# Optimization experiments

Hardware: AMD Instinct MI355X
Metric: run time of the kernel (lower is better)

Reference implementation:

```python
import jax, jax.numpy as jnp
import numpy as np

FG_THRESH = 0.5

def _descriptors(fmap, scribbles):
    # fmap: [B, C, h, w]; scribbles: [B, I, H, W]
    B, C, h, w = fmap.shape
    I = scribbles.shape[1]
    # bilinear resize (align_corners=False == half-pixel, no antialias, like torch)
    sr = jax.image.resize(scribbles, (B, I, h, w), method='bilinear', antialias=False)
    mask = (sr > FG_THRESH).astype(fmap.dtype)                 # [B, I, h, w]
    cnt = mask.sum(axis=(-1, -2))                              # [B, I]
    ssum = jnp.einsum('bihw,bchw->bic', mask, fmap)            # masked sum over HW
    mean = ssum / jnp.maximum(cnt, 1.0)[..., None]             # [B, I, C]
    # fallback when a mask has no foreground pixels: feature at argmax of soft mask
    idx = jnp.argmax(sr.reshape(B, I, h * w), axis=-1)         # [B, I]
    fflat = fmap.reshape(B, C, h * w)
    fb = jnp.take_along_axis(fflat, idx[:, None, :], axis=2)   # [B, C, I]
    fb = fb.transpose(0, 2, 1)                                 # [B, I, C]
    return jnp.where((cnt > 0)[..., None], mean, fb)

def setup_inputs() -> dict:
    key = jax.random.key(0)
    k0, k1, k2, k3 = jax.random.split(key, 4)
    return {
        'feat0': jax.random.normal(k0, (8, 256, 128, 128), dtype=jnp.float32),
        'feat1': jax.random.normal(k1, (8, 256, 64, 64), dtype=jnp.float32),
        'feat2': jax.random.normal(k2, (8, 256, 32, 32), dtype=jnp.float32),
        'scribbles': jax.random.uniform(k3, (8, 16, 512, 512), dtype=jnp.float32),
    }

def reference(feat0, feat1, feat2, scribbles):
    # multi_scale=True, random_bg_queries=False: per-level masked mean pool,
    # then average descriptors across feature levels. Output: [B, I, C]
    d0 = _descriptors(feat0, scribbles)
    d1 = _descriptors(feat1, scribbles)
    d2 = _descriptors(feat2, scribbles)
    return (d0 + d1 + d2) / 3.0
```

## Files before the change

### kernel.cpp

```cpp
#include <hip/hip_runtime.h>
#include <stdint.h>

#define NB 8
#define NI 16
#define NC 256
#define SH 512
#define NCH 84

typedef __bf16 bf16x8 __attribute__((ext_vector_type(8)));
typedef float f32x4 __attribute__((ext_vector_type(4)));
typedef uint32_t u32x4 __attribute__((ext_vector_type(4)));

static const size_t OFF_SSP = 0;
static const size_t OFF_CNT = OFF_SSP + (size_t)NB * NCH * NI * NC * 4;
static const size_t OFF_KEY = OFF_CNT + (size_t)NB * NCH * NI * 4;
static const size_t WS_NEED = OFF_KEY + (size_t)NB * NCH * NI * 8;

__device__ __forceinline__ float4 ld4(const float* p) {
    return *reinterpret_cast<const float4*>(p);
}

__device__ __forceinline__ void mfma_step1(const uint16_t* __restrict__ lmp, int ks, int cl,
                                           const float4 (&buf)[2], f32x4& a0) {
    const uint4 wA = *reinterpret_cast<const uint4*>(lmp + ks * 32);
    u32x4 au;
    au.x = ((wA.x >> cl) & 0x10001u) * 0x3F80u;
    au.y = ((wA.y >> cl) & 0x10001u) * 0x3F80u;
    au.z = ((wA.z >> cl) & 0x10001u) * 0x3F80u;
    au.w = ((wA.w >> cl) & 0x10001u) * 0x3F80u;
    const bf16x8 av = __builtin_bit_cast(bf16x8, au);
    bf16x8 bv;
    bv[0] = (__bf16)buf[0].x; bv[1] = (__bf16)buf[0].y;
    bv[2] = (__bf16)buf[0].z; bv[3] = (__bf16)buf[0].w;
    bv[4] = (__bf16)buf[1].x; bv[5] = (__bf16)buf[1].y;
    bv[6] = (__bf16)buf[1].z; bv[7] = (__bf16)buf[1].w;
    a0 = __builtin_amdgcn_mfma_f32_16x16x32_bf16(av, bv, a0, 0, 0, 0);
}

template<int W, int S, int P>
__device__ __forceinline__ void do_chunk(const float* __restrict__ f,
                                         const float* __restrict__ scr,
                                         float* __restrict__ ssp,
                                         int* __restrict__ cntp,
                                         unsigned long long* __restrict__ keyp,
                                         int b, int chunk, int slot, int tid,
                                         uint8_t* __restrict__ lmask8,
                                         uint16_t* __restrict__ lmask16,
                                         int* __restrict__ lcnt,
                                         unsigned long long* __restrict__ lkey) {
    const int wave = tid >> 6;
    const int lane = tid & 63;
    const int kg = lane >> 4;
    const int cl = lane & 15;
    const int c0 = wave * 16;
    const int kb = chunk * 256;
    const float* fp0 = f + ((size_t)b * NC + c0 + cl) * P + kb + kg * 8;
    float4 bA[2], bB[2];
    bA[0] = ld4(fp0);
    bA[1] = ld4(fp0 + 4);

    const int gi = tid >> 8;
    const int p = tid & 255;
    const int pix = chunk * 256 + p;
    const int y = pix / W;
    const int x = pix - y * W;
    const int r0 = S * y + (S / 2 - 1);
    const int c0s = S * x + (S / 2 - 1);
    const float* sb = scr + ((size_t)b * NI + gi * 4) * (SH * SH) + (size_t)r0 * SH;
    float s4v[4];
    if constexpr (S == 4) {
        float4 q0[4], q1[4];
        #pragma unroll
        for (int i = 0; i < 4; ++i) {
            const float* sp = sb + (size_t)i * (SH * SH);
            q0[i] = ld4(sp + (c0s - 1));
            q1[i] = ld4(sp + SH + (c0s - 1));
        }
        #pragma unroll
        for (int i = 0; i < 4; ++i)
            s4v[i] = (q0[i].y + q0[i].z) + (q1[i].y + q1[i].z);
    } else {
        float qa[4], qb[4], qc[4], qd[4];
        #pragma unroll
        for (int i = 0; i < 4; ++i) {
            const float* sp = sb + (size_t)i * (SH * SH);
            qa[i] = sp[c0s];
            qb[i] = sp[c0s + 1];
            qc[i] = sp[SH + c0s];
            qd[i] = sp[SH + c0s + 1];
        }
        #pragma unroll
        for (int i = 0; i < 4; ++i)
            s4v[i] = (qa[i] + qb[i]) + (qc[i] + qd[i]);
    }
    unsigned int mword = 0;
    #pragma unroll
    for (int i = 0; i < 4; ++i) {
        const float s4 = s4v[i];
        bool bit = s4 > 2.0f;
        mword |= bit ? (1u << i) : 0u;
        unsigned long long bal = __ballot(bit);
        if (lane == 0) atomicAdd(&lcnt[gi * 4 + i], (int)__popcll(bal));
        if (bal == 0ull) {
            unsigned int srb = __float_as_uint(0.25f * s4);
            unsigned int mx = srb;
            #pragma unroll
            for (int off = 1; off < 64; off <<= 1) {
                unsigned int o = __shfl_xor(mx, off, 64);
                mx = (o > mx) ? o : mx;
            }
            unsigned long long win = __ballot(srb == mx);
            if (lane == 0) {
                int wl = __ffsll((unsigned long long)win) - 1;
                unsigned int wpix = (unsigned int)(chunk * 256 + (p & ~63) + wl);
                unsigned long long key = (((unsigned long long)mx) << 32)
                                       | (unsigned long long)(0xFFFFFFFFu - wpix);
                atomicMax(&lkey[gi * 4 + i], key);
            }
        }
    }
    lmask8[gi * 256 + p] = (uint8_t)mword;
    __syncthreads();
    if (tid < 256)
        lmask16[tid] = (uint16_t)((unsigned)lmask8[tid]
                                | ((unsigned)lmask8[256 + tid] << 4)
                                | ((unsigned)lmask8[512 + tid] << 8)
                                | ((unsigned)lmask8[768 + tid] << 12));
    if (tid < NI) {
        cntp[slot * NI + tid] = lcnt[tid];
        keyp[slot * NI + tid] = lkey[tid];
    }
    __syncthreads();

    const uint16_t* lmp = lmask16 + kg * 8;
    f32x4 acc = {0.f, 0.f, 0.f, 0.f};
    #pragma unroll
    for (int ks = 0; ks < 8; ks += 2) {
        {
            const float* fr = fp0 + (ks + 1) * 32;
            bB[0] = ld4(fr);
            bB[1] = ld4(fr + 4);
        }
        mfma_step1(lmp, ks, cl, bA, acc);
        if (ks + 2 < 8) {
            const float* fr = fp0 + (ks + 2) * 32;
            bA[0] = ld4(fr);
            bA[1] = ld4(fr + 4);
        }
        mfma_step1(lmp, ks + 1, cl, bB, acc);
    }
    float* sb2 = ssp + (size_t)slot * (NI * NC);
    const int c = c0 + cl;
    #pragma unroll
    for (int r = 0; r < 4; ++r)
        sb2[(kg * 4 + r) * NC + c] = acc[r];
}

__global__ __launch_bounds__(1024, 8) void fused_kernel(const float* __restrict__ f0,
                                                        const float* __restrict__ f1,
                                                        const float* __restrict__ f2,
                                                        const float* __restrict__ scr,
                                                        float* __restrict__ ssp,
                                                        int* __restrict__ cntp,
                                                        unsigned long long* __restrict__ keyp) {
    __shared__ uint8_t lmask8[1024];
    __shared__ __align__(16) uint16_t lmask16[256];
    __shared__ int lcnt[NI];
    __shared__ unsigned long long lkey[NI];
    const int tid = threadIdx.x;
    const int b = blockIdx.y;
    const int bx = blockIdx.x;
    if (tid < NI) { lcnt[tid] = 0; lkey[tid] = 0ull; }
    __syncthreads();
    const int slot = b * NCH + bx;
    if (bx < 64) {
        do_chunk<128, 4, 16384>(f0, scr, ssp, cntp, keyp, b, bx, slot, tid,
                                lmask8, lmask16, lcnt, lkey);
    } else if (bx < 80) {
        do_chunk<64, 8, 4096>(f1, scr, ssp, cntp, keyp, b, bx - 64, slot, tid,
                              lmask8, lmask16, lcnt, lkey);
    } else {
        do_chunk<32, 16, 1024>(f2, scr, ssp, cntp, keyp, b, bx - 80, slot, tid,
                               lmask8, lmask16, lcnt, lkey);
    }
}

__global__ __launch_bounds__(256) void final_kernel(const float* __restrict__ f0,
                                                    const float* __restrict__ f1,
                                                    const float* __restrict__ f2,
                                                    const int* __restrict__ cntp,
                                                    const unsigned long long* __restrict__ keyp,
                                                    const float* __restrict__ ssp,
                                                    float* __restrict__ out) {
    __shared__ int scnt[3];
    __shared__ unsigned long long skey[3];
    __shared__ float red[4][64];
    const int bi = blockIdx.x;
    const int cq = blockIdx.y;
    const int b = bi >> 4;
    const int i = bi & 15;
    const int tid = threadIdx.x;
    const int cl = tid & 63;
    const int jg = tid >> 6;
    const int CH[3] = {64, 16, 4};
    const int O[3] = {0, 64, 80};
    if (tid < 3) { scnt[tid] = 0; skey[tid] = 0ull; }
    __syncthreads();
    if (tid < NCH) {
        int l = (tid < 64) ? 0 : (tid < 80) ? 1 : 2;
        const int slot = b * NCH + tid;
        atomicAdd(&scnt[l], cntp[slot * NI + i]);
        atomicMax(&skey[l], keyp[slot * NI + i]);
    }
    __syncthreads();
    const float* fl[3] = {f0, f1, f2};
    const int Ps[3] = {16384, 4096, 1024};
    float r = 0.f;
    #pragma unroll
    for (int l = 0; l < 3; ++l) {
        const int cn = scnt[l];
        if (cn > 0) {
            float s = 0.f;
            for (int j = jg; j < CH[l]; j += 4)
                s += ssp[((size_t)(b * NCH + O[l] + j) * NI + i) * NC + cq * 64 + cl];
            red[jg][cl] = s;
            __syncthreads();
            if (jg == 0)
                r += ((red[0][cl] + red[1][cl]) + (red[2][cl] + red[3][cl])) / (float)cn;
            __syncthreads();
        } else if (jg == 0) {
            unsigned int p = 0xFFFFFFFFu - (unsigned int)(skey[l] & 0xFFFFFFFFull);
            r += fl[l][((size_t)b * NC + cq * 64 + cl) * Ps[l] + p];
        }
    }
    if (jg == 0) out[(size_t)bi * NC + cq * 64 + cl] = r * (1.f / 3.f);
}

extern "C" void kernel_launch(void* const* d_in, const int* in_sizes, int n_in,
                              void* d_out, int out_size, void* d_ws, size_t ws_size,
                              hipStream_t stream) {
    const float* f0  = (const float*)d_in[0];
    const float* f1  = (const float*)d_in[1];
    const float* f2  = (const float*)d_in[2];
    const float* scr = (const float*)d_in[3];
    float* out = (float*)d_out;
    char* ws = (char*)d_ws;
    if (ws_size < WS_NEED) return;

    float* ssp = (float*)(ws + OFF_SSP);
    int* cntp = (int*)(ws + OFF_CNT);
    unsigned long long* keyp = (unsigned long long*)(ws + OFF_KEY);

    fused_kernel<<<dim3(NCH, NB), 1024, 0, stream>>>(f0, f1, f2, scr, ssp, cntp, keyp);
    final_kernel<<<dim3(NB * NI, 4), 256, 0, stream>>>(f0, f1, f2, cntp, keyp, ssp, out);
}
```

Before: 64.07 us.

## Accumulate per-level partial sums with global atomics instead of per-chunk slots

Each chunk block now adds its masked sums, counts and argmax keys straight into one small per-level, per-batch buffer using atomics, instead of writing a separate per-chunk slot. The final kernel then only divides and picks the fallback, with no reduction over chunks. This removes the large partial-sum write and read-back (about 5.5 MB). In exchange it adds a zeroing kernel launch, contended float atomics on the same addresses from up to 64 blocks, and a summation order that is no longer deterministic.

```diff
diff --git a/kernel.cpp b/kernel.cpp
--- a/kernel.cpp
+++ b/kernel.cpp
@@ -11,13 +11,19 @@
 typedef float f32x4 __attribute__((ext_vector_type(4)));
 typedef uint32_t u32x4 __attribute__((ext_vector_type(4)));
 
-static const size_t OFF_SSP = 0;
-static const size_t OFF_CNT = OFF_SSP + (size_t)NB * NCH * NI * NC * 4;
-static const size_t OFF_KEY = OFF_CNT + (size_t)NB * NCH * NI * 4;
-static const size_t WS_NEED = OFF_KEY + (size_t)NB * NCH * NI * 8;
+static const size_t OFF_SSUM = 0;
+static const size_t OFF_CNT  = OFF_SSUM + (size_t)3 * NB * NI * NC * 4;
+static const size_t OFF_KEY  = OFF_CNT + (size_t)3 * NB * NI * 4;
+static const size_t WS_NEED  = OFF_KEY + (size_t)3 * NB * NI * 8;
+static const int    ZERO_N4  = (int)(WS_NEED / 16);
 
 __device__ __forceinline__ float4 ld4(const float* p) {
     return *reinterpret_cast<const float4*>(p);
+}
+
+__global__ __launch_bounds__(256) void zero_kernel(float4* __restrict__ ws4) {
+    const int i = blockIdx.x * 256 + threadIdx.x;
+    if (i < ZERO_N4) ws4[i] = make_float4(0.f, 0.f, 0.f, 0.f);
 }
 
 __device__ __forceinline__ void mfma_step1(const uint16_t* __restrict__ lmp, int ks, int cl,
@@ -40,10 +46,10 @@
 template<int W, int S, int P>
 __device__ __forceinline__ void do_chunk(const float* __restrict__ f,
                                          const float* __restrict__ scr,
-                                         float* __restrict__ ssp,
-                                         int* __restrict__ cntp,
-                                         unsigned long long* __restrict__ keyp,
-                                         int b, int chunk, int slot, int tid,
+                                         float* __restrict__ ssum_lb,
+                                         int* __restrict__ cnt_lb,
+                                         unsigned long long* __restrict__ key_lb,
+                                         int b, int chunk, int tid,
                                          uint8_t* __restrict__ lmask8,
                                          uint16_t* __restrict__ lmask16,
                                          int* __restrict__ lcnt,
@@ -127,8 +133,10 @@
                                 | ((unsigned)lmask8[512 + tid] << 8)
                                 | ((unsigned)lmask8[768 + tid] << 12));
     if (tid < NI) {
-        cntp[slot * NI + tid] = lcnt[tid];
-        keyp[slot * NI + tid] = lkey[tid];
+        int v = lcnt[tid];
+        if (v) atomicAdd(&cnt_lb[tid], v);
+        unsigned long long k = lkey[tid];
+        if (k) atomicMax(&key_lb[tid], k);
     }
     __syncthreads();
 
@@ -149,20 +157,19 @@
         }
         mfma_step1(lmp, ks + 1, cl, bB, acc);
     }
-    float* sb2 = ssp + (size_t)slot * (NI * NC);
     const int c = c0 + cl;
     #pragma unroll
     for (int r = 0; r < 4; ++r)
-        sb2[(kg * 4 + r) * NC + c] = acc[r];
+        atomicAdd(&ssum_lb[(kg * 4 + r) * NC + c], acc[r]);
 }
 
 __global__ __launch_bounds__(1024, 8) void fused_kernel(const float* __restrict__ f0,
                                                         const float* __restrict__ f1,
                                                         const float* __restrict__ f2,
                                                         const float* __restrict__ scr,
-                                                        float* __restrict__ ssp,
-                                                        int* __restrict__ cntp,
-                                                        unsigned long long* __restrict__ keyp) {
+                                                        float* __restrict__ ssum,
+                                                        int* __restrict__ cnt,
+                                                        unsigned long long* __restrict__ key) {
     __shared__ uint8_t lmask8[1024];
     __shared__ __align__(16) uint16_t lmask16[256];
     __shared__ int lcnt[NI];
@@ -172,68 +179,48 @@
     const int bx = blockIdx.x;
     if (tid < NI) { lcnt[tid] = 0; lkey[tid] = 0ull; }
     __syncthreads();
-    const int slot = b * NCH + bx;
     if (bx < 64) {
-        do_chunk<128, 4, 16384>(f0, scr, ssp, cntp, keyp, b, bx, slot, tid,
-                                lmask8, lmask16, lcnt, lkey);
+        const size_t o = (size_t)(0 * NB + b);
+        do_chunk<128, 4, 16384>(f0, scr, ssum + o * NI * NC, cnt + o * NI, key + o * NI,
+                                b, bx, tid, lmask8, lmask16, lcnt, lkey);
     } else if (bx < 80) {
-        do_chunk<64, 8, 4096>(f1, scr, ssp, cntp, keyp, b, bx - 64, slot, tid,
-                              lmask8, lmask16, lcnt, lkey);
+        const size_t o = (size_t)(1 * NB + b);
+        do_chunk<64, 8, 4096>(f1, scr, ssum + o * NI * NC, cnt + o * NI, key + o * NI,
+                              b, bx - 64, tid, lmask8, lmask16, lcnt, lkey);
     } else {
-        do_chunk<32, 16, 1024>(f2, scr, ssp, cntp, keyp, b, bx - 80, slot, tid,
-                               lmask8, lmask16, lcnt, lkey);
+        const size_t o = (size_t)(2 * NB + b);
+        do_chunk<32, 16, 1024>(f2, scr, ssum + o * NI * NC, cnt + o * NI, key + o * NI,
+                               b, bx - 80, tid, lmask8, lmask16, lcnt, lkey);
     }
 }
 
 __global__ __launch_bounds__(256) void final_kernel(const float* __restrict__ f0,
                                                     const float* __restrict__ f1,
                                                     const float* __restrict__ f2,
-                                                    const int* __restrict__ cntp,
-                                                    const unsigned long long* __restrict__ keyp,
-                                                    const float* __restrict__ ssp,
+                                                    const int* __restrict__ cnt,
+                                                    const unsigned long long* __restrict__ key,
+                                                    const float* __restrict__ ssum,
                                                     float* __restrict__ out) {
-    __shared__ int scnt[3];
-    __shared__ unsigned long long skey[3];
-    __shared__ float red[4][64];
     const int bi = blockIdx.x;
-    const int cq = blockIdx.y;
+    const int c = threadIdx.x;
     const int b = bi >> 4;
-    const int i = bi & 15;
-    const int tid = threadIdx.x;
-    const int cl = tid & 63;
-    const int jg = tid >> 6;
-    const int CH[3] = {64, 16, 4};
-    const int O[3] = {0, 64, 80};
-    if (tid < 3) { scnt[tid] = 0; skey[tid] = 0ull; }
-    __syncthreads();
-    if (tid < NCH) {
-        int l = (tid < 64) ? 0 : (tid < 80) ? 1 : 2;
-        const int slot = b * NCH + tid;
-        atomicAdd(&scnt[l], cntp[slot * NI + i]);
-        atomicMax(&skey[l], keyp[slot * NI + i]);
-    }
-    __syncthreads();
     const float* fl[3] = {f0, f1, f2};
     const int Ps[3] = {16384, 4096, 1024};
     float r = 0.f;
     #pragma unroll
     for (int l = 0; l < 3; ++l) {
-        const int cn = scnt[l];
+        const int cn = cnt[l * NB * NI + bi];
+        float v;
         if (cn > 0) {
-            float s = 0.f;
-            for (int j = jg; j < CH[l]; j += 4)
-                s += ssp[((size_t)(b * NCH + O[l] + j) * NI + i) * NC + cq * 64 + cl];
-            red[jg][cl] = s;
-            __syncthreads();
-            if (jg == 0)
-                r += ((red[0][cl] + red[1][cl]) + (red[2][cl] + red[3][cl])) / (float)cn;
-            __syncthreads();
-        } else if (jg == 0) {
-            unsigned int p = 0xFFFFFFFFu - (unsigned int)(skey[l] & 0xFFFFFFFFull);
-            r += fl[l][((size_t)b * NC + cq * 64 + cl) * Ps[l] + p];
-        }
-    }
-    if (jg == 0) out[(size_t)bi * NC + cq * 64 + cl] = r * (1.f / 3.f);
+            v = ssum[((size_t)l * NB * NI + bi) * NC + c] / (float)cn;
+        } else {
+            unsigned int p = 0xFFFFFFFFu -
+                (unsigned int)(key[l * NB * NI + bi] & 0xFFFFFFFFull);
+            v = fl[l][((size_t)b * NC + c) * Ps[l] + p];
+        }
+        r += v;
+    }
+    out[(size_t)bi * NC + c] = r * (1.f / 3.f);
 }
 
 extern "C" void kernel_launch(void* const* d_in, const int* in_sizes, int n_in,
@@ -247,10 +234,11 @@
     char* ws = (char*)d_ws;
     if (ws_size < WS_NEED) return;
 
-    float* ssp = (float*)(ws + OFF_SSP);
-    int* cntp = (int*)(ws + OFF_CNT);
-    unsigned long long* keyp = (unsigned long long*)(ws + OFF_KEY);
-
-    fused_kernel<<<dim3(NCH, NB), 1024, 0, stream>>>(f0, f1, f2, scr, ssp, cntp, keyp);
-    final_kernel<<<dim3(NB * NI, 4), 256, 0, stream>>>(f0, f1, f2, cntp, keyp, ssp, out);
-}
+    float* ssum = (float*)(ws + OFF_SSUM);
+    int* cnt = (int*)(ws + OFF_CNT);
+    unsigned long long* key = (unsigned long long*)(ws + OFF_KEY);
+
+    zero_kernel<<<(ZERO_N4 + 255) / 256, 256, 0, stream>>>((float4*)ws);
+    fused_kernel<<<dim3(NCH, NB), 1024, 0, stream>>>(f0, f1, f2, scr, ssum, cnt, key);
+    final_kernel<<<NB * NI, NC, 0, stream>>>(f0, f1, f2, cnt, key, ssum, out);
+}
```

Measured after the change: 61.72 us. 1.04x faster.
